# Optimization experiments

Measured on AMD Instinct MI355X. Metric: run time of the kernel, lower is better.

The kernel has to match this reference:

```python
import jax, jax.numpy as jnp
import numpy as np

# static config (matches init_kwargs)
H, W = 56, 56
T = 4            # temporal_dims
C = 256          # dim1
NH = 8           # num_heads
WS = 7           # window_size
SS = 3           # shift_size
HID = 1024       # mlp hidden = 4*C
N = WS * WS      # tokens per window
EPS = 1e-5


def _ln(x, g, b):
    m = jnp.mean(x, axis=-1, keepdims=True)
    v = jnp.mean((x - m) ** 2, axis=-1, keepdims=True)
    return (x - m) * jax.lax.rsqrt(v + EPS) * g + b


def _window_partition(x, ws):
    B, Hh, Ww, Cc = x.shape
    x = x.reshape(B, Hh // ws, ws, Ww // ws, ws, Cc)
    return x.transpose(0, 1, 3, 2, 4, 5).reshape(-1, ws, ws, Cc)


def _window_reverse(win, ws, Hh, Ww):
    B = win.shape[0] // ((Hh // ws) * (Ww // ws))
    x = win.reshape(B, Hh // ws, Ww // ws, ws, ws, -1)
    return x.transpose(0, 1, 3, 2, 4, 5).reshape(B, Hh, Ww, -1)


def _rel_pos_index(ws):
    coords = np.stack(np.meshgrid(np.arange(ws), np.arange(ws), indexing='ij'))
    cf = coords.reshape(2, -1)
    rel = (cf[:, :, None] - cf[:, None, :]).transpose(1, 2, 0).astype(np.int64)
    rel[..., 0] += ws - 1
    rel[..., 1] += ws - 1
    rel[..., 0] *= 2 * ws - 1
    return rel.sum(-1)  # (ws*ws, ws*ws)


def _shift_mask():
    # identical to the torch buffer built in __init__ (on temporal_dims*H x W grid)
    img = np.zeros((T * H, W), dtype=np.float32)
    cnt = 0
    for hs in (slice(0, -WS), slice(-WS, -SS), slice(-SS, None)):
        for wsl in (slice(0, -WS), slice(-WS, -SS), slice(-SS, None)):
            img[hs, wsl] = cnt
            cnt += 1
    mw = img.reshape((T * H) // WS, WS, W // WS, WS).transpose(0, 2, 1, 3).reshape(-1, N)
    am = mw[:, None, :] - mw[:, :, None]
    return np.where(am != 0, np.float32(-100.0), np.float32(0.0))  # (nW, N, N)

_RPI = _rel_pos_index(WS)
_ATTN_MASK = _shift_mask()


def setup_inputs() -> dict:
    key = jax.random.key(0)
    ks = jax.random.split(key, 8)
    B = 4
    s = 0.02
    return {
        'x1': jax.random.normal(ks[0], (B, T * H * W, C), jnp.float32),
        'x2': jax.random.normal(ks[1], (B, H * W, C), jnp.float32),
        'norm1_g': jnp.ones((C,), jnp.float32),
        'norm1_b': jnp.zeros((C,), jnp.float32),
        'qkv_w': jax.random.normal(ks[2], (3 * C, C), jnp.float32) * s,
        'qkv_b': jnp.zeros((3 * C,), jnp.float32),
        'proj_w': jax.random.normal(ks[3], (C, C), jnp.float32) * s,
        'proj_b': jnp.zeros((C,), jnp.float32),
        'rpb_table': jax.random.normal(ks[4], ((2 * WS - 1) ** 2, NH), jnp.float32) * s,
        'norm2_g': jnp.ones((C,), jnp.float32),
        'norm2_b': jnp.zeros((C,), jnp.float32),
        'fc1_w': jax.random.normal(ks[5], (HID, C), jnp.float32) * s,
        'fc1_b': jnp.zeros((HID,), jnp.float32),
        'fc2_w': jax.random.normal(ks[6], (C, HID), jnp.float32) * s,
        'fc2_b': jnp.zeros((C,), jnp.float32),
    }


def _block(x1, norm1_g, norm1_b, qkv_w, qkv_b, proj_w, proj_b, rpb_table,
           norm2_g, norm2_b, fc1_w, fc1_b, fc2_w, fc2_b):
    B, L, _ = x1.shape
    hd = C // NH
    shortcut = x1
    x = _ln(x1, norm1_g, norm1_b).reshape(B, T * H, W, C)
    # cyclic shift + window partition
    x = jnp.roll(x, shift=(-SS, -SS), axis=(1, 2))
    xw = _window_partition(x, WS).reshape(-1, N, C)          # (B*nW, N, C)
    Bw = xw.shape[0]
    nW = Bw // B
    # window attention with relative position bias + shift mask
    qkv = (xw @ qkv_w.T + qkv_b).reshape(Bw, N, 3, NH, hd).transpose(2, 0, 3, 1, 4)
    q, k, v = qkv[0], qkv[1], qkv[2]
    attn = jnp.einsum('bhnd,bhmd->bhnm', q * (hd ** -0.5), k)
    bias = rpb_table[jnp.asarray(_RPI)].transpose(2, 0, 1)    # (NH, N, N)
    attn = attn + bias[None]
    mask = jnp.asarray(_ATTN_MASK)
    attn = attn.reshape(B, nW, NH, N, N) + mask[None, :, None]
    attn = jax.nn.softmax(attn.reshape(Bw, NH, N, N), axis=-1)
    y = jnp.einsum('bhnm,bhmd->bhnd', attn, v).transpose(0, 2, 1, 3).reshape(Bw, N, C)
    y = y @ proj_w.T + proj_b
    # reverse windows + un-shift
    y = _window_reverse(y.reshape(-1, WS, WS, C), WS, T * H, W)
    y = jnp.roll(y, shift=(SS, SS), axis=(1, 2)).reshape(B, L, C)
    out = y
    x1 = shortcut + y
    # MLP (GELU exact, as torch nn.GELU default)
    h = _ln(x1, norm2_g, norm2_b)
    h = jax.nn.gelu(h @ fc1_w.T + fc1_b, approximate=False)
    x1 = x1 + (h @ fc2_w.T + fc2_b)
    return x1, out


def reference(x1, x2, norm1_g, norm1_b, qkv_w, qkv_b, proj_w, proj_b, rpb_table,
              norm2_g, norm2_b, fc1_w, fc1_b, fc2_w, fc2_b):
    # last_view=True: x2 is reshaped but unused by the executed path
    return _block(x1, norm1_g, norm1_b, qkv_w, qkv_b, proj_w, proj_b, rpb_table,
                  norm2_g, norm2_b, fc1_w, fc1_b, fc2_w, fc2_b)
```

## Files before the change

### kernel.cpp

```cpp
#include <hip/hip_runtime.h>
#include <hip/hip_bf16.h>
#include <cmath>

#define CDIM 256
#define TPW 49
#define NWIN 1024
#define MTOK (NWIN * TPW)
#define NHEAD 8
#define GH 224
#define GW 56
#define PLD 72

typedef __attribute__((ext_vector_type(8))) __bf16 bf16x8;
typedef __attribute__((ext_vector_type(4))) float f32x4;

__device__ __forceinline__ __bf16 to_bf16(float f) {
    __hip_bfloat16 h = __float2bfloat16(f);
    return *(__bf16*)&h;
}

__device__ __forceinline__ void async_copy16(const void* g, void* l) {
    __builtin_amdgcn_global_load_lds(
        (const __attribute__((address_space(1))) void*)g,
        (__attribute__((address_space(3))) void*)l, 16, 0, 0);
}

__device__ __forceinline__ float wave_sum(float v) {
    v += __shfl_down(v, 32);
    v += __shfl_down(v, 16);
    v += __shfl_down(v, 8);
    v += __shfl_down(v, 4);
    v += __shfl_down(v, 2);
    v += __shfl_down(v, 1);
    return v;
}

__global__ __launch_bounds__(256) void castall_kernel(
    const float* __restrict__ qw, const float* __restrict__ pw,
    const float* __restrict__ f1, const float* __restrict__ f2,
    __hip_bfloat16* __restrict__ dst)
{
    const int i = blockIdx.x * 256 + threadIdx.x;
    float v;
    if (i < 196608) v = qw[i];
    else if (i < 262144) v = pw[i - 196608];
    else if (i < 524288) v = f1[i - 262144];
    else v = f2[i - 524288];
    dst[i] = __float2bfloat16(v);
}

__global__ __launch_bounds__(256) void cb_kernel(
    const float* __restrict__ rpb, float* __restrict__ cbt)
{
    const int cls = blockIdx.x >> 3, head = blockIdx.x & 7;
    for (int e = threadIdx.x; e < 64 * 64; e += 256) {
        const int m = e >> 6, n = e & 63;
        float v;
        if (m >= 49 || n >= 49) v = -30000.0f;
        else {
            const int in_ = n / 7, jn = n - in_ * 7;
            const int im = m / 7, jm = m - im * 7;
            v = rpb[((in_ - im + 6) * 13 + (jn - jm + 6)) * 8 + head];
            const int hn = (cls & 2) ? 217 + in_ : in_;
            const int wn = (cls & 1) ? 49 + jn : jn;
            const int hm = (cls & 2) ? 217 + im : im;
            const int wm = (cls & 1) ? 49 + jm : jm;
            const int rn = (hn < 217 ? 0 : (hn < 221 ? 3 : 6)) + (wn < 49 ? 0 : (wn < 53 ? 1 : 2));
            const int rm = (hm < 217 ? 0 : (hm < 221 ? 3 : 6)) + (wm < 49 ? 0 : (wm < 53 ? 1 : 2));
            if (rn != rm) v -= 100.0f;
        }
        cbt[((long)blockIdx.x * 64 + m) * 64 + n] = v;
    }
}

__global__ __launch_bounds__(256) void ln1_window_kernel(
    const float* __restrict__ x1, const float* __restrict__ g,
    const float* __restrict__ b, __hip_bfloat16* __restrict__ out)
{
    const int wave = threadIdx.x >> 6, lane = threadIdx.x & 63;
    const int t = blockIdx.x * 4 + wave;
    const int bw = t / TPW, n = t - bw * TPW;
    const int bb = bw >> 8, wi = bw & 255;
    const int hb = wi >> 3, wb = wi & 7;
    const int i = n / 7, j = n - i * 7;
    int h0 = hb * 7 + i + 3; if (h0 >= GH) h0 -= GH;
    int w0 = wb * 7 + j + 3; if (w0 >= GW) w0 -= GW;
    const long src = ((long)(bb * GH + h0) * GW + w0) * CDIM + lane * 4;
    const float4 v = *(const float4*)(x1 + src);
    float s = v.x + v.y + v.z + v.w;
    s = wave_sum(s);
    const float mean = __shfl(s, 0) * (1.0f / 256.0f);
    const float4 d = { v.x - mean, v.y - mean, v.z - mean, v.w - mean };
    float s2 = d.x * d.x + d.y * d.y + d.z * d.z + d.w * d.w;
    s2 = wave_sum(s2);
    const float rstd = rsqrtf(__shfl(s2, 0) * (1.0f / 256.0f) + 1e-5f);
    const float4 g4 = *(const float4*)(g + lane * 4);
    const float4 b4 = *(const float4*)(b + lane * 4);
    short4 pk;
    { __bf16 h = to_bf16(d.x * rstd * g4.x + b4.x); pk.x = *(short*)&h; }
    { __bf16 h = to_bf16(d.y * rstd * g4.y + b4.y); pk.y = *(short*)&h; }
    { __bf16 h = to_bf16(d.z * rstd * g4.z + b4.z); pk.z = *(short*)&h; }
    { __bf16 h = to_bf16(d.w * rstd * g4.w + b4.w); pk.w = *(short*)&h; }
    *(short4*)((short*)out + (long)t * CDIM + lane * 4) = pk;
}

__global__ __launch_bounds__(256) void ln_kernel(
    const float* __restrict__ x, const float* __restrict__ g,
    const float* __restrict__ b, __hip_bfloat16* __restrict__ out)
{
    const int wave = threadIdx.x >> 6, lane = threadIdx.x & 63;
    const long t = (long)blockIdx.x * 4 + wave;
    const float4 v = *(const float4*)(x + t * CDIM + lane * 4);
    float s = v.x + v.y + v.z + v.w;
    s = wave_sum(s);
    const float mean = __shfl(s, 0) * (1.0f / 256.0f);
    const float4 d = { v.x - mean, v.y - mean, v.z - mean, v.w - mean };
    float s2 = d.x * d.x + d.y * d.y + d.z * d.z + d.w * d.w;
    s2 = wave_sum(s2);
    const float rstd = rsqrtf(__shfl(s2, 0) * (1.0f / 256.0f) + 1e-5f);
    const float4 g4 = *(const float4*)(g + lane * 4);
    const float4 b4 = *(const float4*)(b + lane * 4);
    short4 pk;
    { __bf16 h = to_bf16(d.x * rstd * g4.x + b4.x); pk.x = *(short*)&h; }
    { __bf16 h = to_bf16(d.y * rstd * g4.y + b4.y); pk.y = *(short*)&h; }
    { __bf16 h = to_bf16(d.z * rstd * g4.z + b4.z); pk.z = *(short*)&h; }
    { __bf16 h = to_bf16(d.w * rstd * g4.w + b4.w); pk.w = *(short*)&h; }
    *(short4*)((short*)out + t * CDIM + lane * 4) = pk;
}

template <int EPI, typename OutT>
__global__ __launch_bounds__(256) void gemm_mfma(
    const __hip_bfloat16* __restrict__ X, const __hip_bfloat16* __restrict__ W,
    const float* __restrict__ bias, OutT* __restrict__ Y,
    int M, int K, int N, const float* __restrict__ res, float* __restrict__ Y2)
{
    __shared__ __hip_bfloat16 As[128 * 32];
    __shared__ __hip_bfloat16 Bs[128 * 32];
    const int tid = threadIdx.x;
    const int wave = tid >> 6, lane = tid & 63;
    const int nwg = gridDim.x * gridDim.y;
    const int L = blockIdx.y * gridDim.x + blockIdx.x;
    const int cpx = nwg >> 3;
    const int orig = (L & 7) * cpx + (L >> 3);
    const int bxx = orig % gridDim.x;
    const int byy = orig / gridDim.x;
    const int bm = byy * 128, bn = bxx * 128;
    const int wm = (wave & 1) * 64, wn = (wave >> 1) * 64;
    const int m16 = lane & 15, quad = lane >> 4;
    const int srow = lane >> 2;
    const int scol = (lane & 3) * 8;

    f32x4 acc[4][4] = {};

    for (int k0 = 0; k0 < K; k0 += 32) {
#pragma unroll
        for (int j = 0; j < 2; ++j) {
            const int rg = wave * 2 + j;
            const int row = rg * 16 + srow;
            async_copy16(X + (long)(bm + row) * K + k0 + scol, (char*)As + rg * 1024);
            async_copy16(W + (long)(bn + row) * K + k0 + scol, (char*)Bs + rg * 1024);
        }
        __syncthreads();
        bf16x8 af[4], bf[4];
#pragma unroll
        for (int i = 0; i < 4; ++i)
            af[i] = *(const bf16x8*)&As[(wm + i * 16 + m16) * 32 + quad * 8];
#pragma unroll
        for (int j = 0; j < 4; ++j)
            bf[j] = *(const bf16x8*)&Bs[(wn + j * 16 + m16) * 32 + quad * 8];
#pragma unroll
        for (int i = 0; i < 4; ++i)
#pragma unroll
            for (int j = 0; j < 4; ++j)
                acc[i][j] = __builtin_amdgcn_mfma_f32_16x16x32_bf16(bf[j], af[i], acc[i][j], 0, 0, 0);
        __syncthreads();
    }

#pragma unroll
    for (int i = 0; i < 4; ++i) {
        const long row = bm + wm + i * 16 + m16;
        long drow = row;
        if (EPI == 3) {
            const unsigned t = (unsigned)row;
            const unsigned bw_ = t / 49u;
            const unsigned n_ = t - bw_ * 49u;
            const unsigned bb = bw_ >> 8, wi = bw_ & 255u;
            const unsigned hb = wi >> 3, wbl = wi & 7u;
            const unsigned ii = n_ / 7u, jj = n_ - ii * 7u;
            int h0 = hb * 7 + ii + 3; if (h0 >= GH) h0 -= GH;
            int w0 = wbl * 7 + jj + 3; if (w0 >= GW) w0 -= GW;
            drow = (long)bb * (GH * GW) + h0 * GW + w0;
        }
#pragma unroll
        for (int j = 0; j < 4; ++j) {
            const int col = bn + wn + j * 16 + quad * 4;
            const float4 b4 = *(const float4*)&bias[col];
            float v[4];
            v[0] = acc[i][j][0] + b4.x;
            v[1] = acc[i][j][1] + b4.y;
            v[2] = acc[i][j][2] + b4.z;
            v[3] = acc[i][j][3] + b4.w;
            if (EPI == 1) {
#pragma unroll
                for (int r = 0; r < 4; ++r)
                    v[r] = 0.5f * v[r] * (1.0f + erff(v[r] * 0.70710678118654752f));
            }
            if (EPI == 0 || EPI == 1) {
                short4 pk;
                { __bf16 h = to_bf16(v[0]); pk.x = *(short*)&h; }
                { __bf16 h = to_bf16(v[1]); pk.y = *(short*)&h; }
                { __bf16 h = to_bf16(v[2]); pk.z = *(short*)&h; }
                { __bf16 h = to_bf16(v[3]); pk.w = *(short*)&h; }
                *(short4*)((short*)Y + row * N + col) = pk;
            } else if (EPI == 2) {
                const float4 r4 = *(const float4*)(res + row * N + col);
                float4 o4 = { v[0] + r4.x, v[1] + r4.y, v[2] + r4.z, v[3] + r4.w };
                *(float4*)((float*)Y + row * N + col) = o4;
            } else if (EPI == 3) {
                const long a = drow * 256 + col;
                const float4 x4 = *(const float4*)(res + a);
                float4 y4 = { v[0], v[1], v[2], v[3] };
                *(float4*)(Y2 + a) = y4;
                float4 s4 = { v[0] + x4.x, v[1] + x4.y, v[2] + x4.z, v[3] + x4.w };
                *(float4*)((float*)Y + a) = s4;
            }
        }
    }
}

__global__ __launch_bounds__(256) void fused_mlp_kernel(
    const __hip_bfloat16* __restrict__ A,
    const __hip_bfloat16* __restrict__ W1,
    const float* __restrict__ b1,
    const __hip_bfloat16* __restrict__ W2,
    const float* __restrict__ b2,
    float* __restrict__ io)
{
    __shared__ __hip_bfloat16 Wbuf[16384];
    __shared__ char Hb[8192];
    const int tid = threadIdx.x;
    const int wave = tid >> 6, lane = tid & 63;
    const int m16 = lane & 15, quad = lane >> 4;
    const int L = blockIdx.x;
    const int orig = (L & 7) * 98 + (L >> 3);
    const long bm = (long)orig * 64;

    const int lr = wave * 16 + m16;
    const int swz = (lr & 7) << 4;

    bf16x8 af[8];
    const __hip_bfloat16* arow = A + (bm + lr) * 256 + quad * 8;
#pragma unroll
    for (int kk = 0; kk < 8; ++kk)
        af[kk] = *(const bf16x8*)(arow + kk * 32);

    f32x4 acc2[16] = {};

    for (int c = 0; c < 16; ++c) {
        {
            const __hip_bfloat16* src = W1 + (long)c * 64 * 256;
#pragma unroll
            for (int r = 0; r < 8; ++r) {
                const int s = (tid << 4) + (r << 12);
                const int row = s >> 9;
                const int g = ((s >> 4) & 31) ^ (row & 7);
                async_copy16(src + row * 256 + g * 8,
                             (char*)Wbuf + (r << 12) + wave * 1024);
            }
        }
        __syncthreads();
        f32x4 s1[4] = {};
#pragma unroll
        for (int kk = 0; kk < 8; ++kk) {
#pragma unroll
            for (int j = 0; j < 4; ++j) {
                const int n = j * 16 + m16;
                const int off = n * 512 + ((kk * 64 + quad * 16) ^ ((n & 7) << 4));
                const bf16x8 wf = *(const bf16x8*)((const char*)Wbuf + off);
                s1[j] = __builtin_amdgcn_mfma_f32_16x16x32_bf16(wf, af[kk], s1[j], 0, 0, 0);
            }
        }
        __syncthreads();
        {
            const __hip_bfloat16* src = W2 + c * 64;
#pragma unroll
            for (int r = 0; r < 8; ++r) {
                const int s = (tid << 4) + (r << 12);
                const int row = s >> 7;
                const int g = ((s >> 4) & 7) ^ (row & 7);
                async_copy16(src + (long)row * 1024 + g * 8,
                             (char*)Wbuf + (r << 12) + wave * 1024);
            }
        }
#pragma unroll
        for (int j = 0; j < 4; ++j) {
            const float4 bb = *(const float4*)(b1 + c * 64 + j * 16 + quad * 4);
            float v[4];
            v[0] = s1[j][0] + bb.x; v[1] = s1[j][1] + bb.y;
            v[2] = s1[j][2] + bb.z; v[3] = s1[j][3] + bb.w;
#pragma unroll
            for (int r = 0; r < 4; ++r)
                v[r] = 0.5f * v[r] * (1.0f + erff(v[r] * 0.70710678118654752f));
            short4 pk;
            { __bf16 h = to_bf16(v[0]); pk.x = *(short*)&h; }
            { __bf16 h = to_bf16(v[1]); pk.y = *(short*)&h; }
            { __bf16 h = to_bf16(v[2]); pk.z = *(short*)&h; }
            { __bf16 h = to_bf16(v[3]); pk.w = *(short*)&h; }
            const int off = lr * 128 + ((j * 32 + quad * 8) ^ swz);
            *(short4*)(Hb + off) = pk;
        }
        __syncthreads();
#pragma unroll
        for (int kk = 0; kk < 2; ++kk) {
            const int hoff = lr * 128 + ((kk * 64 + quad * 16) ^ swz);
            const bf16x8 hf = *(const bf16x8*)(Hb + hoff);
#pragma unroll
            for (int f = 0; f < 16; ++f) {
                const int nn = f * 16 + m16;
                const int off = nn * 128 + ((kk * 64 + quad * 16) ^ ((nn & 7) << 4));
                const bf16x8 wf = *(const bf16x8*)((const char*)Wbuf + off);
                acc2[f] = __builtin_amdgcn_mfma_f32_16x16x32_bf16(wf, hf, acc2[f], 0, 0, 0);
            }
        }
        __syncthreads();
    }

    const long grow = bm + lr;
#pragma unroll
    for (int f = 0; f < 16; ++f) {
        const int col = f * 16 + quad * 4;
        const float4 bb = *(const float4*)(b2 + col);
        const long a = grow * 256 + col;
        const float4 r4 = *(const float4*)(io + a);
        float4 o4 = { acc2[f][0] + bb.x + r4.x, acc2[f][1] + bb.y + r4.y,
                      acc2[f][2] + bb.z + r4.z, acc2[f][3] + bb.w + r4.w };
        *(float4*)(io + a) = o4;
    }
}

__global__ __launch_bounds__(256) void attn_mfma_kernel(
    const __hip_bfloat16* __restrict__ qkv,
    const float* __restrict__ cbt,
    __hip_bfloat16* __restrict__ yout)
{
    __shared__ __bf16 P[4][64][PLD];
    const int tid = threadIdx.x;
    const int wave = tid >> 6, lane = tid & 63;
    const int bw = blockIdx.x >> 1;
    const int head = (blockIdx.x & 1) * 4 + wave;
    const int m16 = lane & 15, quad = lane >> 4;
    const int wi = bw & 255;
    const int hb = wi >> 3, wb = wi & 7;
    const int cls = ((hb == 31) ? 2 : 0) + ((wb == 7) ? 1 : 0);

    const __bf16* qb = (const __bf16*)qkv + (long)bw * TPW * 768 + head * 32;

    bf16x8 qf[4], kf[4];
#pragma unroll
    for (int i = 0; i < 4; ++i) {
        const int n = i * 16 + m16;
        bf16x8 q = {}, k = {};
        if (n < TPW) {
            const __bf16* p = qb + (long)n * 768 + quad * 8;
            q = *(const bf16x8*)p;
            k = *(const bf16x8*)(p + 256);
        }
        qf[i] = q; kf[i] = k;
    }

    bf16x8 vf[2][2];
#pragma unroll
    for (int jt = 0; jt < 2; ++jt)
#pragma unroll
        for (int kt = 0; kt < 2; ++kt) {
            bf16x8 v = {};
#pragma unroll
            for (int j = 0; j < 8; ++j) {
                const int tok = kt * 32 + quad * 8 + j;
                if (tok < TPW) v[j] = qb[(long)tok * 768 + 512 + jt * 16 + m16];
            }
            vf[jt][kt] = v;
        }

    f32x4 s[4][4] = {};
#pragma unroll
    for (int i = 0; i < 4; ++i)
#pragma unroll
        for (int j = 0; j < 4; ++j)
            s[i][j] = __builtin_amdgcn_mfma_f32_16x16x32_bf16(qf[i], kf[j], s[i][j], 0, 0, 0);

    const float* cb = cbt + (long)(cls * 8 + head) * 64 * 64;
#pragma unroll
    for (int j = 0; j < 4; ++j) {
        const int m = j * 16 + m16;
#pragma unroll
        for (int i = 0; i < 4; ++i) {
            const float4 c = *(const float4*)(cb + m * 64 + i * 16 + quad * 4);
            s[i][j][0] = s[i][j][0] * 0.17677669529663687f + c.x;
            s[i][j][1] = s[i][j][1] * 0.17677669529663687f + c.y;
            s[i][j][2] = s[i][j][2] * 0.17677669529663687f + c.z;
            s[i][j][3] = s[i][j][3] * 0.17677669529663687f + c.w;
        }
    }

#pragma unroll
    for (int i = 0; i < 4; ++i) {
#pragma unroll
        for (int r = 0; r < 4; ++r) {
            float mx = fmaxf(fmaxf(s[i][0][r], s[i][1][r]), fmaxf(s[i][2][r], s[i][3][r]));
            mx = fmaxf(mx, __shfl_xor(mx, 1));
            mx = fmaxf(mx, __shfl_xor(mx, 2));
            mx = fmaxf(mx, __shfl_xor(mx, 4));
            mx = fmaxf(mx, __shfl_xor(mx, 8));
            float sum = 0.0f;
#pragma unroll
            for (int j = 0; j < 4; ++j) {
                const float e = __expf(s[i][j][r] - mx);
                s[i][j][r] = e;
                sum += e;
            }
            sum += __shfl_xor(sum, 1);
            sum += __shfl_xor(sum, 2);
            sum += __shfl_xor(sum, 4);
            sum += __shfl_xor(sum, 8);
            const float inv = 1.0f / sum;
#pragma unroll
            for (int j = 0; j < 4; ++j)
                P[wave][i * 16 + quad * 4 + r][j * 16 + m16] = to_bf16(s[i][j][r] * inv);
        }
    }

    f32x4 o[4][2] = {};
#pragma unroll
    for (int kt = 0; kt < 2; ++kt)
#pragma unroll
        for (int i = 0; i < 4; ++i) {
            const bf16x8 pf = *(const bf16x8*)&P[wave][i * 16 + m16][kt * 32 + quad * 8];
#pragma unroll
            for (int jt = 0; jt < 2; ++jt)
                o[i][jt] = __builtin_amdgcn_mfma_f32_16x16x32_bf16(vf[jt][kt], pf, o[i][jt], 0, 0, 0);
        }

#pragma unroll
    for (int i = 0; i < 4; ++i) {
        const int tok = i * 16 + m16;
        if (tok < TPW) {
#pragma unroll
            for (int jt = 0; jt < 2; ++jt) {
                short4 pk;
                { __bf16 h = to_bf16(o[i][jt][0]); pk.x = *(short*)&h; }
                { __bf16 h = to_bf16(o[i][jt][1]); pk.y = *(short*)&h; }
                { __bf16 h = to_bf16(o[i][jt][2]); pk.z = *(short*)&h; }
                { __bf16 h = to_bf16(o[i][jt][3]); pk.w = *(short*)&h; }
                *(short4*)((short*)yout + ((long)bw * TPW + tok) * CDIM + head * 32 + jt * 16 + quad * 4) = pk;
            }
        }
    }
}

extern "C" void kernel_launch(void* const* d_in, const int* in_sizes, int n_in,
                              void* d_out, int out_size, void* d_ws, size_t ws_size,
                              hipStream_t stream) {
    (void)in_sizes; (void)n_in; (void)out_size; (void)ws_size;
    const float* x1     = (const float*)d_in[0];
    const float* n1g    = (const float*)d_in[2];
    const float* n1b    = (const float*)d_in[3];
    const float* qkv_w  = (const float*)d_in[4];
    const float* qkv_b  = (const float*)d_in[5];
    const float* proj_w = (const float*)d_in[6];
    const float* proj_b = (const float*)d_in[7];
    const float* rpb    = (const float*)d_in[8];
    const float* n2g    = (const float*)d_in[9];
    const float* n2b    = (const float*)d_in[10];
    const float* fc1_w  = (const float*)d_in[11];
    const float* fc1_b  = (const float*)d_in[12];
    const float* fc2_w  = (const float*)d_in[13];
    const float* fc2_b  = (const float*)d_in[14];

    float* out_x1 = (float*)d_out;
    float* out_y  = out_x1 + (long)MTOK * CDIM;

    char* ws = (char*)d_ws;
    const size_t SZ_A   = (size_t)MTOK * CDIM * sizeof(__hip_bfloat16);
    const size_t SZ_BIG = (size_t)MTOK * 1024 * sizeof(__hip_bfloat16);
    __hip_bfloat16* A    = (__hip_bfloat16*)ws;
    char*           BIG  = ws + SZ_A;
    __hip_bfloat16* qkvb = (__hip_bfloat16*)BIG;
    __hip_bfloat16* wB   = (__hip_bfloat16*)(ws + SZ_A + SZ_BIG);
    __hip_bfloat16* qkv_wb  = wB;
    __hip_bfloat16* proj_wb = wB + 196608;
    __hip_bfloat16* fc1_wb  = wB + 262144;
    __hip_bfloat16* fc2_wb  = wB + 524288;
    float* cbt = (float*)(wB + 786432);

    castall_kernel<<<3072, 256, 0, stream>>>(qkv_w, proj_w, fc1_w, fc2_w, wB);
    cb_kernel<<<32, 256, 0, stream>>>(rpb, cbt);
    ln1_window_kernel<<<MTOK / 4, 256, 0, stream>>>(x1, n1g, n1b, A);
    gemm_mfma<0, __hip_bfloat16><<<dim3(768 / 128, MTOK / 128), 256, 0, stream>>>(
        A, qkv_wb, qkv_b, qkvb, MTOK, CDIM, 768, nullptr, nullptr);
    attn_mfma_kernel<<<NWIN * 2, 256, 0, stream>>>(qkvb, cbt, A);
    gemm_mfma<3, float><<<dim3(256 / 128, MTOK / 128), 256, 0, stream>>>(
        A, proj_wb, proj_b, out_x1, MTOK, CDIM, CDIM, x1, out_y);
    ln_kernel<<<MTOK / 4, 256, 0, stream>>>(out_x1, n2g, n2b, A);
    fused_mlp_kernel<<<MTOK / 64, 256, 0, stream>>>(
        A, fc1_wb, fc1_b, fc2_wb, fc2_b, out_x1);
}
```

Measured before the change: 477.2 us.

## Double M-tile in fused MLP, split W1/W2 buffers, pass GELU output via shuffles

The fused MLP kernel now processes 128 rows per block (two 16-row tiles per wave), so each weight fragment read from LDS feeds two MFMAs. W1 and W2 chunks get separate LDS buffers, and the next chunk is prefetched while the current one is consumed, which removes a barrier per iteration. The GELU hidden activations are moved into MFMA operand layout with cross-lane shuffles instead of an LDS round trip. This costs more registers (acc2 doubles to 32 f32x4, held at 2 blocks/CU) and halves the grid to 392 blocks, which may leave some CUs underused.

```diff
diff --git a/kernel.cpp b/kernel.cpp
--- a/kernel.cpp
+++ b/kernel.cpp
@@ -17,6 +17,12 @@
 __device__ __forceinline__ __bf16 to_bf16(float f) {
     __hip_bfloat16 h = __float2bfloat16(f);
     return *(__bf16*)&h;
+}
+
+__device__ __forceinline__ unsigned pack2(float a, float b) {
+    __hip_bfloat16 ha = __float2bfloat16(a);
+    __hip_bfloat16 hb = __float2bfloat16(b);
+    return (unsigned)*(unsigned short*)&ha | ((unsigned)*(unsigned short*)&hb << 16);
 }
 
 __device__ __forceinline__ void async_copy16(const void* g, void* l) {
@@ -228,7 +234,7 @@
     }
 }
 
-__global__ __launch_bounds__(256) void fused_mlp_kernel(
+__global__ __launch_bounds__(256, 2) void fused_mlp_kernel(
     const __hip_bfloat16* __restrict__ A,
     const __hip_bfloat16* __restrict__ W1,
     const float* __restrict__ b1,
@@ -236,105 +242,144 @@
     const float* __restrict__ b2,
     float* __restrict__ io)
 {
-    __shared__ __hip_bfloat16 Wbuf[16384];
-    __shared__ char Hb[8192];
+    __shared__ __hip_bfloat16 W1buf[16384];
+    __shared__ __hip_bfloat16 W2buf[16384];
     const int tid = threadIdx.x;
     const int wave = tid >> 6, lane = tid & 63;
     const int m16 = lane & 15, quad = lane >> 4;
     const int L = blockIdx.x;
-    const int orig = (L & 7) * 98 + (L >> 3);
-    const long bm = (long)orig * 64;
-
-    const int lr = wave * 16 + m16;
-    const int swz = (lr & 7) << 4;
-
-    bf16x8 af[8];
-    const __hip_bfloat16* arow = A + (bm + lr) * 256 + quad * 8;
-#pragma unroll
-    for (int kk = 0; kk < 8; ++kk)
-        af[kk] = *(const bf16x8*)(arow + kk * 32);
-
-    f32x4 acc2[16] = {};
+    const int orig = (L & 7) * 49 + (L >> 3);
+    const long bm = (long)orig * 128;
+
+    const int selhi = (lane >> 5) & 1;
+    const int lA = ((lane & 16) << 1) | (lane & 15);
+
+    bf16x8 af[2][8];
+#pragma unroll
+    for (int m = 0; m < 2; ++m) {
+        const __hip_bfloat16* arow = A + (bm + wave * 32 + m * 16 + m16) * 256 + quad * 8;
+#pragma unroll
+        for (int kk = 0; kk < 8; ++kk)
+            af[m][kk] = *(const bf16x8*)(arow + kk * 32);
+    }
+
+    {
+        const __hip_bfloat16* src = W1;
+#pragma unroll
+        for (int r = 0; r < 8; ++r) {
+            const int s = (tid << 4) + (r << 12);
+            const int row = s >> 9;
+            const int g = ((s >> 4) & 31) ^ (row & 7);
+            async_copy16(src + row * 256 + g * 8, (char*)W1buf + (r << 12) + wave * 1024);
+        }
+        const __hip_bfloat16* src2 = W2;
+#pragma unroll
+        for (int r = 0; r < 8; ++r) {
+            const int s = (tid << 4) + (r << 12);
+            const int row = s >> 7;
+            const int g = ((s >> 4) & 7) ^ (row & 7);
+            async_copy16(src2 + (long)row * 1024 + g * 8, (char*)W2buf + (r << 12) + wave * 1024);
+        }
+    }
+    __syncthreads();
+
+    f32x4 acc2[2][16] = {};
 
     for (int c = 0; c < 16; ++c) {
-        {
-            const __hip_bfloat16* src = W1 + (long)c * 64 * 256;
+        f32x4 s1[2][4] = {};
+#pragma unroll
+        for (int kk = 0; kk < 8; ++kk) {
+#pragma unroll
+            for (int j = 0; j < 4; ++j) {
+                const int n = j * 16 + m16;
+                const int off = n * 512 + ((kk * 64 + quad * 16) ^ ((n & 7) << 4));
+                const bf16x8 wf = *(const bf16x8*)((const char*)W1buf + off);
+                s1[0][j] = __builtin_amdgcn_mfma_f32_16x16x32_bf16(wf, af[0][kk], s1[0][j], 0, 0, 0);
+                s1[1][j] = __builtin_amdgcn_mfma_f32_16x16x32_bf16(wf, af[1][kk], s1[1][j], 0, 0, 0);
+            }
+        }
+        unsigned pkl[2][4], pkh[2][4];
+#pragma unroll
+        for (int m = 0; m < 2; ++m)
+#pragma unroll
+            for (int j = 0; j < 4; ++j) {
+                const float4 bb = *(const float4*)(b1 + c * 64 + j * 16 + quad * 4);
+                float v[4];
+                v[0] = s1[m][j][0] + bb.x; v[1] = s1[m][j][1] + bb.y;
+                v[2] = s1[m][j][2] + bb.z; v[3] = s1[m][j][3] + bb.w;
+#pragma unroll
+                for (int r = 0; r < 4; ++r)
+                    v[r] = 0.5f * v[r] * (1.0f + erff(v[r] * 0.70710678118654752f));
+                pkl[m][j] = pack2(v[0], v[1]);
+                pkh[m][j] = pack2(v[2], v[3]);
+            }
+        __syncthreads();
+        if (c < 15) {
+            const __hip_bfloat16* src = W1 + (long)(c + 1) * 64 * 256;
 #pragma unroll
             for (int r = 0; r < 8; ++r) {
                 const int s = (tid << 4) + (r << 12);
                 const int row = s >> 9;
                 const int g = ((s >> 4) & 31) ^ (row & 7);
-                async_copy16(src + row * 256 + g * 8,
-                             (char*)Wbuf + (r << 12) + wave * 1024);
+                async_copy16(src + row * 256 + g * 8, (char*)W1buf + (r << 12) + wave * 1024);
+            }
+        }
+#pragma unroll
+        for (int kk2 = 0; kk2 < 2; ++kk2) {
+            bf16x8 hf[2];
+#pragma unroll
+            for (int m = 0; m < 2; ++m) {
+                const int ja = kk2 * 2, jb = ja + 1;
+                const unsigned va_lo = __shfl(pkl[m][ja], lA);
+                const unsigned vb_lo = __shfl(pkl[m][jb], lA);
+                const unsigned va_hi = __shfl(pkh[m][ja], lA);
+                const unsigned vb_hi = __shfl(pkh[m][jb], lA);
+                const unsigned wa_lo = __shfl(pkl[m][ja], lA + 16);
+                const unsigned wb_lo = __shfl(pkl[m][jb], lA + 16);
+                const unsigned wa_hi = __shfl(pkh[m][ja], lA + 16);
+                const unsigned wb_hi = __shfl(pkh[m][jb], lA + 16);
+                union { int4 i; bf16x8 v; } u;
+                u.i.x = selhi ? (int)vb_lo : (int)va_lo;
+                u.i.y = selhi ? (int)vb_hi : (int)va_hi;
+                u.i.z = selhi ? (int)wb_lo : (int)wa_lo;
+                u.i.w = selhi ? (int)wb_hi : (int)wa_hi;
+                hf[m] = u.v;
+            }
+#pragma unroll
+            for (int f = 0; f < 16; ++f) {
+                const int nn = f * 16 + m16;
+                const int off = nn * 128 + ((kk2 * 64 + quad * 16) ^ ((nn & 7) << 4));
+                const bf16x8 wf = *(const bf16x8*)((const char*)W2buf + off);
+                acc2[0][f] = __builtin_amdgcn_mfma_f32_16x16x32_bf16(wf, hf[0], acc2[0][f], 0, 0, 0);
+                acc2[1][f] = __builtin_amdgcn_mfma_f32_16x16x32_bf16(wf, hf[1], acc2[1][f], 0, 0, 0);
             }
         }
         __syncthreads();
-        f32x4 s1[4] = {};
-#pragma unroll
-        for (int kk = 0; kk < 8; ++kk) {
-#pragma unroll
-            for (int j = 0; j < 4; ++j) {
-                const int n = j * 16 + m16;
-                const int off = n * 512 + ((kk * 64 + quad * 16) ^ ((n & 7) << 4));
-                const bf16x8 wf = *(const bf16x8*)((const char*)Wbuf + off);
-                s1[j] = __builtin_amdgcn_mfma_f32_16x16x32_bf16(wf, af[kk], s1[j], 0, 0, 0);
-            }
-        }
-        __syncthreads();
-        {
-            const __hip_bfloat16* src = W2 + c * 64;
+        if (c < 15) {
+            const __hip_bfloat16* src2 = W2 + (c + 1) * 64;
 #pragma unroll
             for (int r = 0; r < 8; ++r) {
                 const int s = (tid << 4) + (r << 12);
                 const int row = s >> 7;
                 const int g = ((s >> 4) & 7) ^ (row & 7);
-                async_copy16(src + (long)row * 1024 + g * 8,
-                             (char*)Wbuf + (r << 12) + wave * 1024);
-            }
-        }
-#pragma unroll
-        for (int j = 0; j < 4; ++j) {
-            const float4 bb = *(const float4*)(b1 + c * 64 + j * 16 + quad * 4);
-            float v[4];
-            v[0] = s1[j][0] + bb.x; v[1] = s1[j][1] + bb.y;
-            v[2] = s1[j][2] + bb.z; v[3] = s1[j][3] + bb.w;
-#pragma unroll
-            for (int r = 0; r < 4; ++r)
-                v[r] = 0.5f * v[r] * (1.0f + erff(v[r] * 0.70710678118654752f));
-            short4 pk;
-            { __bf16 h = to_bf16(v[0]); pk.x = *(short*)&h; }
-            { __bf16 h = to_bf16(v[1]); pk.y = *(short*)&h; }
-            { __bf16 h = to_bf16(v[2]); pk.z = *(short*)&h; }
-            { __bf16 h = to_bf16(v[3]); pk.w = *(short*)&h; }
-            const int off = lr * 128 + ((j * 32 + quad * 8) ^ swz);
-            *(short4*)(Hb + off) = pk;
-        }
-        __syncthreads();
-#pragma unroll
-        for (int kk = 0; kk < 2; ++kk) {
-            const int hoff = lr * 128 + ((kk * 64 + quad * 16) ^ swz);
-            const bf16x8 hf = *(const bf16x8*)(Hb + hoff);
-#pragma unroll
-            for (int f = 0; f < 16; ++f) {
-                const int nn = f * 16 + m16;
-                const int off = nn * 128 + ((kk * 64 + quad * 16) ^ ((nn & 7) << 4));
-                const bf16x8 wf = *(const bf16x8*)((const char*)Wbuf + off);
-                acc2[f] = __builtin_amdgcn_mfma_f32_16x16x32_bf16(wf, hf, acc2[f], 0, 0, 0);
-            }
-        }
-        __syncthreads();
-    }
-
-    const long grow = bm + lr;
-#pragma unroll
-    for (int f = 0; f < 16; ++f) {
-        const int col = f * 16 + quad * 4;
-        const float4 bb = *(const float4*)(b2 + col);
-        const long a = grow * 256 + col;
-        const float4 r4 = *(const float4*)(io + a);
-        float4 o4 = { acc2[f][0] + bb.x + r4.x, acc2[f][1] + bb.y + r4.y,
-                      acc2[f][2] + bb.z + r4.z, acc2[f][3] + bb.w + r4.w };
-        *(float4*)(io + a) = o4;
+                async_copy16(src2 + (long)row * 1024 + g * 8, (char*)W2buf + (r << 12) + wave * 1024);
+            }
+        }
+    }
+
+#pragma unroll
+    for (int m = 0; m < 2; ++m) {
+        const long grow = bm + wave * 32 + m * 16 + m16;
+#pragma unroll
+        for (int f = 0; f < 16; ++f) {
+            const int col = f * 16 + quad * 4;
+            const float4 bb = *(const float4*)(b2 + col);
+            const long a = grow * 256 + col;
+            const float4 r4 = *(const float4*)(io + a);
+            float4 o4 = { acc2[m][f][0] + bb.x + r4.x, acc2[m][f][1] + bb.y + r4.y,
+                          acc2[m][f][2] + bb.z + r4.z, acc2[m][f][3] + bb.w + r4.w };
+            *(float4*)(io + a) = o4;
+        }
     }
 }
 
@@ -502,6 +547,6 @@
     gemm_mfma<3, float><<<dim3(256 / 128, MTOK / 128), 256, 0, stream>>>(
         A, proj_wb, proj_b, out_x1, MTOK, CDIM, CDIM, x1, out_y);
     ln_kernel<<<MTOK / 4, 256, 0, stream>>>(out_x1, n2g, n2b, A);
-    fused_mlp_kernel<<<MTOK / 64, 256, 0, stream>>>(
+    fused_mlp_kernel<<<MTOK / 128, 256, 0, stream>>>(
         A, fc1_wb, fc1_b, fc2_wb, fc2_b, out_x1);
 }
```

Result: slower. 663.8 us (+39.1%).
